# Kernel tuning notes

Measured on AMD Instinct MI355X. Metric: run time of the kernel, lower is better.

Reference implementation:

```python
import jax, jax.numpy as jnp
import numpy as np

HEAD_SIZE = 128
LAMBDA_INIT = 0.8
FILL = 1e-09  # the module fills masked positions with 1e-9 (not -inf); reproduce faithfully


def setup_inputs() -> dict:
    key = jax.random.key(0)
    ks = jax.random.split(key, 12)
    B, T, C = 8, 2048, 1024
    q = jax.random.normal(ks[0], (B, T, C), dtype=jnp.float32)
    k = jax.random.normal(ks[1], (B, T, C), dtype=jnp.float32)
    v = jax.random.normal(ks[2], (B, T, C), dtype=jnp.float32)
    pad_mask = jax.random.randint(ks[3], (B, T), 0, 2, dtype=jnp.int32)
    scale = 1.0 / np.sqrt(C)
    Wq = jax.random.normal(ks[4], (C, 2 * HEAD_SIZE), dtype=jnp.float32) * scale
    Wk = jax.random.normal(ks[5], (C, 2 * HEAD_SIZE), dtype=jnp.float32) * scale
    Wv = jax.random.normal(ks[6], (C, HEAD_SIZE), dtype=jnp.float32) * scale
    lq1 = jax.random.normal(ks[7], (HEAD_SIZE,), dtype=jnp.float32)
    lk1 = jax.random.normal(ks[8], (HEAD_SIZE,), dtype=jnp.float32)
    lq2 = jax.random.normal(ks[9], (HEAD_SIZE,), dtype=jnp.float32)
    lk2 = jax.random.normal(ks[10], (HEAD_SIZE,), dtype=jnp.float32)
    return {"q": q, "k": k, "v": v, "pad_mask": pad_mask,
            "Wq": Wq, "Wk": Wk, "Wv": Wv,
            "lq1": lq1, "lk1": lk1, "lq2": lq2, "lk2": lk2}


def reference(q, k, v, pad_mask, Wq, Wk, Wv, lq1, lk1, lq2, lk2):
    B, T_q, C = q.shape
    T_k = k.shape[1]
    Q = q @ Wq                      # [B, Tq, 2*hs]
    K = k @ Wk                      # [B, Tk, 2*hs]
    V = v @ Wv                      # [B, Tk, ho]
    Q1, Q2 = jnp.split(Q, 2, axis=-1)
    K1, K2 = jnp.split(K, 2, axis=-1)
    s1 = jnp.einsum("bqd,bkd->bqk", Q1, K1)
    s2 = jnp.einsum("bqd,bkd->bqk", Q2, K2)
    # causal mask: tril(ones, diagonal=1) == 0 -> fill (note diagonal=1, one lookahead)
    causal_fill = jnp.tril(jnp.ones((T_q, T_k), dtype=bool), 1) == False
    s1 = jnp.where(causal_fill[None], FILL, s1)
    s2 = jnp.where(causal_fill[None], FILL, s2)
    # pad mask broadcast over the KEY axis per query row (as in original)
    pad_fill = (pad_mask == 1)[:, :, None]  # [B, Tq, 1]
    s1 = jnp.where(pad_fill, FILL, s1)
    s2 = jnp.where(pad_fill, FILL, s2)
    scale = HEAD_SIZE ** (-0.5)
    lbd = jnp.exp(jnp.dot(lq1, lk1)) - jnp.exp(jnp.dot(lq2, lk2)) + LAMBDA_INIT
    attn = jax.nn.softmax(s1 * scale, axis=-1) - lbd * jax.nn.softmax(s2 * scale, axis=-1)
    return attn @ V                 # [B, Tq, ho]
```

## Files before the change

kernel.cpp:

```cpp
#include <hip/hip_runtime.h>
#include <math.h>


#define T_SEQ 2048
#define NB 8
#define CDIM 1024
#define HS 128

constexpr float SCALE = 0.08838834764831845f;

typedef float f32x4 __attribute__((ext_vector_type(4)));
typedef __bf16 bf16x8 __attribute__((ext_vector_type(8)));
typedef unsigned int u32;

#define MFMA16 __builtin_amdgcn_mfma_f32_16x16x32_bf16

__device__ __forceinline__ void gld16(const void* g, void* l) {
  __builtin_amdgcn_global_load_lds(
      (const __attribute__((address_space(1))) u32*)g,
      (__attribute__((address_space(3))) u32*)l, 16, 0, 0);
}

__device__ __forceinline__ void wg_barrier_lds() {
  asm volatile("s_waitcnt lgkmcnt(0)" ::: "memory");
  __builtin_amdgcn_s_barrier();
  __builtin_amdgcn_sched_barrier(0);
}

__device__ __forceinline__ bf16x8 cvt8(f32x4 lo, f32x4 hi) {
  bf16x8 r;
  r[0] = (__bf16)lo.x; r[1] = (__bf16)lo.y; r[2] = (__bf16)lo.z; r[3] = (__bf16)lo.w;
  r[4] = (__bf16)hi.x; r[5] = (__bf16)hi.y; r[6] = (__bf16)hi.z; r[7] = (__bf16)hi.w;
  return r;
}

__global__ __launch_bounds__(128) void lambda_kernel(
    const float* __restrict__ lq1, const float* __restrict__ lk1,
    const float* __restrict__ lq2, const float* __restrict__ lk2,
    float* __restrict__ lbd) {
  __shared__ float r1[128], r2[128];
  int t = threadIdx.x;
  r1[t] = lq1[t] * lk1[t];
  r2[t] = lq2[t] * lk2[t];
  __syncthreads();
  for (int s = 64; s > 0; s >>= 1) {
    if (t < s) { r1[t] += r1[t + s]; r2[t] += r2[t + s]; }
    __syncthreads();
  }
  if (t == 0) *lbd = expf(r1[0]) - expf(r2[0]) + 0.8f;
}

__global__ __launch_bounds__(256) void pack_w(
    const float* __restrict__ Wq, const float* __restrict__ Wk,
    const float* __restrict__ Wv, __bf16* __restrict__ Wp) {
  int nt = blockIdx.x;
  const float* W; int colbase, N;
  if (nt < 16)      { W = Wq; colbase = nt * 16;        N = 256; }
  else if (nt < 32) { W = Wk; colbase = (nt - 16) * 16; N = 256; }
  else              { W = Wv; colbase = (nt - 32) * 16; N = 128; }
  int tid = threadIdx.x;
#pragma unroll
  for (int i = 0; i < 8; ++i) {
    int u = tid + 256 * i;
    int ks = u >> 6, lane = u & 63;
    int l15 = lane & 15, quad = lane >> 4;
    bf16x8 pk;
#pragma unroll
    for (int j = 0; j < 8; ++j)
      pk[j] = (__bf16)W[(size_t)(ks * 32 + quad * 8 + j) * N + colbase + l15];
    *(bf16x8*)(Wp + ((size_t)(nt * 32 + ks) * 64 + lane) * 8) = pk;
  }
}

template<int NT, int NTG>
__device__ __forceinline__ void proj_body(
    const float* __restrict__ Ablk, const __bf16* __restrict__ Wp,
    __bf16* __restrict__ outp, __bf16* __restrict__ Vt,
    int rows0, char* smem) {
  constexpr int NT2 = NT / 2;
  float*  sA = (float*)smem;
  __bf16* sB = (__bf16*)(smem + 16384);
  const int tid = threadIdx.x;
  const int lane = tid & 63, wave = tid >> 6;
  const int wr = wave >> 1, wc = wave & 1;
  const int l15 = lane & 15, quad = lane >> 4;
  const int arow = lane >> 3;
  const int ac16 = (lane & 7) ^ arow;

  f32x4 acc0[NT2], acc1[NT2];
#pragma unroll
  for (int j = 0; j < NT2; ++j) {
    acc0[j] = (f32x4){0.f, 0.f, 0.f, 0.f};
    acc1[j] = (f32x4){0.f, 0.f, 0.f, 0.f};
  }

  auto stage_ks = [&](int ks, int buf) {
    const float* gA = Ablk + ks * 32;
    float* lA = sA + buf * 2048;
#pragma unroll
    for (int i = 0; i < 2; ++i) {
      int li = wave * 2 + i;
      gld16(gA + (size_t)(li * 8 + arow) * CDIM + ac16 * 4, lA + li * 256);
    }
    __bf16* lB = sB + buf * 8192;
#pragma unroll
    for (int i = 0; i < 4; ++i) {
      int ntl = i * 4 + wave;
      if (ntl < NT)
        gld16(Wp + ((size_t)((NTG + ntl) * 32 + ks) * 64 + lane) * 8,
              lB + ntl * 512);
    }
  };

  stage_ks(0, 0);
  for (int ks = 0; ks < 32; ++ks) {
    const int buf = ks & 1;
    __syncthreads();
    const float* lA = sA + buf * 2048;
    int r0 = wr * 32 + l15;
    f32x4 lo0 = *(const f32x4*)(lA + r0 * 32 + (((quad * 2)     ^ (l15 & 7)) * 4));
    f32x4 hi0 = *(const f32x4*)(lA + r0 * 32 + (((quad * 2 + 1) ^ (l15 & 7)) * 4));
    bf16x8 af0 = cvt8(lo0, hi0);
    int r1 = r0 + 16;
    f32x4 lo1 = *(const f32x4*)(lA + r1 * 32 + (((quad * 2)     ^ (l15 & 7)) * 4));
    f32x4 hi1 = *(const f32x4*)(lA + r1 * 32 + (((quad * 2 + 1) ^ (l15 & 7)) * 4));
    bf16x8 af1 = cvt8(lo1, hi1);
    if (ks < 31) stage_ks(ks + 1, buf ^ 1);
    const __bf16* lB = sB + buf * 8192;
#pragma unroll
    for (int nt = 0; nt < NT2; ++nt) {
      bf16x8 bf = *(const bf16x8*)(lB + (wc * NT2 + nt) * 512 + lane * 8);
      acc0[nt] = MFMA16(af0, bf, acc0[nt], 0, 0, 0);
      acc1[nt] = MFMA16(af1, bf, acc1[nt], 0, 0, 0);
    }
  }

  __syncthreads();
  constexpr int N = NT * 16;
  constexpr int TS = N + 8;
  __bf16* tile = (__bf16*)smem;
#pragma unroll
  for (int ntl = 0; ntl < NT2; ++ntl) {
    f32x4 a0 = acc0[ntl];
    f32x4 a1 = acc1[ntl];
#pragma unroll
    for (int r = 0; r < 4; ++r) {
      tile[(wr * 32 + quad * 4 + r) * TS + (wc * NT2 + ntl) * 16 + l15] = (__bf16)a0[r];
      tile[(wr * 32 + 16 + quad * 4 + r) * TS + (wc * NT2 + ntl) * 16 + l15] = (__bf16)a1[r];
    }
  }
  __syncthreads();
  constexpr int CPR = N / 8;
#pragma unroll
  for (int i = 0; i < (64 * CPR) / 256; ++i) {
    int u = tid + 256 * i;
    int row = u / CPR, c8 = u % CPR;
    bf16x8 val = *(const bf16x8*)(tile + row * TS + c8 * 8);
    *(bf16x8*)(outp + (size_t)(rows0 + row) * N + c8 * 8) = val;
  }
  if constexpr (NT == 8) {
    int b = rows0 >> 11, t0 = rows0 & 2047;
#pragma unroll
    for (int i = 0; i < 4; ++i) {
      int u = tid + 256 * i;
      int tc = u & 7, c = u >> 3;
      bf16x8 pk;
#pragma unroll
      for (int j = 0; j < 8; ++j) pk[j] = tile[(tc * 8 + j) * TS + c];
      *(bf16x8*)(Vt + ((size_t)(b * 128 + c)) * T_SEQ + t0 + tc * 8) = pk;
    }
  }
}

__global__ __launch_bounds__(256, 3) void proj_mfma(
    const float* __restrict__ qin, const float* __restrict__ kin,
    const float* __restrict__ vin, const __bf16* __restrict__ Wp,
    __bf16* __restrict__ Qo, __bf16* __restrict__ Ko,
    __bf16* __restrict__ Vo, __bf16* __restrict__ Vt) {
  __shared__ char smem[49152];
  const int blk = blockIdx.x;
  const int rows0 = (blk & 255) * 64;
  if (blk < 256)
    proj_body<16, 0>(qin + (size_t)rows0 * CDIM, Wp, Qo, nullptr, rows0, smem);
  else if (blk < 512)
    proj_body<16, 16>(kin + (size_t)rows0 * CDIM, Wp, Ko, nullptr, rows0, smem);
  else
    proj_body<8, 32>(vin + (size_t)rows0 * CDIM, Wp, Vo, Vt, rows0, smem);
}

#define VCH 64
#define VCS 32
__global__ __launch_bounds__(128) void vcsum_a(const __bf16* __restrict__ V,
                                               float* __restrict__ csum) {
  int blk = blockIdx.x; int b = blk >> 6, ch = blk & 63;
  int c = threadIdx.x;
  const __bf16* vp = V + ((size_t)b * T_SEQ + ch * VCS) * HS + c;
  float s = 0.f;
#pragma unroll 4
  for (int t = 0; t < VCS; ++t) s += (float)vp[(size_t)t * HS];
  csum[(size_t)blk * HS + c] = s;
}

__global__ __launch_bounds__(128) void vcsum_b(const __bf16* __restrict__ V,
                                               const float* __restrict__ csum,
                                               float* __restrict__ cum) {
  int blk = blockIdx.x; int b = blk >> 6, ch = blk & 63;
  int c = threadIdx.x;
  float run = 0.f;
  for (int j = 0; j < ch; ++j) run += csum[(size_t)(b * VCH + j) * HS + c];
  const __bf16* vp = V + ((size_t)b * T_SEQ + ch * VCS) * HS + c;
  float* cp = cum + ((size_t)b * (T_SEQ + 1) + ch * VCS) * HS + c;
  if (ch == 0) cp[0] = 0.f;
#pragma unroll 4
  for (int t = 0; t < VCS; ++t) {
    run += (float)vp[(size_t)t * HS];
    cp[(size_t)(t + 1) * HS] = run;
  }
}

__global__ __launch_bounds__(512, 2) void attn_mfma(
    const __bf16* __restrict__ Q, const __bf16* __restrict__ K,
    const __bf16* __restrict__ Vt, const float* __restrict__ cum,
    const int* __restrict__ pad, const float* __restrict__ lbdp,
    float* __restrict__ out) {
  __shared__ __bf16 sQ[32 * 264];
  __shared__ __bf16 sK[2][64 * 256];
  __shared__ __bf16 sP[2][2][32 * 72];
  __shared__ float zb[2][32][64];
  __shared__ float zfin[2][32];

  const int tid = threadIdx.x;
  const int lane = tid & 63, wave = tid >> 6;
  const int wm = wave >> 2, wk = wave & 3;
  const int l15 = lane & 15, quad = lane >> 4;

  const int p = blockIdx.x;
  const int b = p & 7;
  const int ti = 63 - (p >> 3);
  const int q0 = ti * 32;
  const float lbd = *lbdp;
  const __bf16* Qb = Q + (size_t)b * T_SEQ * 256;
  const __bf16* Kb = K + (size_t)b * T_SEQ * 256;
  const __bf16* Vtb = Vt + (size_t)b * HS * T_SEQ;
  const float* cumb = cum + (size_t)b * (T_SEQ + 1) * HS;
  const float pc = (1.f - lbd) * (1.f / (float)T_SEQ);

  const int lastkey = q0 + 32;
  const int nkt = (min(lastkey, T_SEQ - 1) >> 6) + 1;

  auto stageK = [&](int k0, int sbuf) {
#pragma unroll
    for (int i = 0; i < 4; ++i) {
      int u = i * 512 + tid;
      int row = u >> 5, c = u & 31;
      int cg = (c & 24) | ((c ^ row) & 7);
      gld16(Kb + (size_t)(k0 + row) * 256 + cg * 8,
            &sK[sbuf][(size_t)(i * 512 + wave * 64) * 8]);
    }
  };

  stageK(0, 0);
#pragma unroll
  for (int i = 0; i < 2; ++i) {
    int c = tid + 512 * i;
    int row = c >> 5, c16 = c & 31;
    *(f32x4*)(&sQ[row * 264 + c16 * 8]) =
        *(const f32x4*)(Qb + (size_t)(q0 + row) * 256 + c16 * 8);
  }
  __syncthreads();

  bf16x8 qf[2][4];
  {
    const int row = wm * 16 + l15;
#pragma unroll
    for (int pl = 0; pl < 2; ++pl)
#pragma unroll
      for (int s = 0; s < 4; ++s)
        qf[pl][s] = *(const bf16x8*)(&sQ[row * 264 + pl * 128 + s * 32 + quad * 8]);
  }

  f32x4 O[2][2];
#pragma unroll
  for (int i = 0; i < 2; ++i)
#pragma unroll
    for (int j = 0; j < 2; ++j) O[i][j] = (f32x4){0.f, 0.f, 0.f, 0.f};
  float z[2][4] = {};

  const int kr = wk * 16 + l15;

  for (int kt = 0; kt < nkt; ++kt) {
    const int k0 = kt << 6;
    const int buf = kt & 1;
    const bool needmask = (k0 + 63 > q0 + 1);

    bf16x8 vf[2][2];
#pragma unroll
    for (int nt = 0; nt < 2; ++nt)
#pragma unroll
      for (int ks = 0; ks < 2; ++ks)
        vf[nt][ks] = *(const bf16x8*)(Vtb + (size_t)(wk * 32 + nt * 16 + l15) * T_SEQ +
                                      k0 + ks * 32 + quad * 8);
    if (kt + 1 < nkt) stageK(k0 + 64, buf ^ 1);

    f32x4 S[2];
#pragma unroll
    for (int mat = 0; mat < 2; ++mat) {
      S[mat] = (f32x4){0.f, 0.f, 0.f, 0.f};
#pragma unroll
      for (int s = 0; s < 4; ++s) {
        int cd = mat * 16 + s * 4 + quad;
        int slot = (cd & 24) | ((cd ^ kr) & 7);
        bf16x8 kfrag = *(const bf16x8*)(&sK[buf][(size_t)kr * 256 + slot * 8]);
        S[mat] = MFMA16(qf[mat][s], kfrag, S[mat], 0, 0, 0);
      }
    }

    const int rowl = wm * 16 + quad * 4;
    const int keyg = k0 + kr;
#pragma unroll
    for (int mat = 0; mat < 2; ++mat)
#pragma unroll
      for (int r = 0; r < 4; ++r) {
        float pv;
        if (needmask) {
          int rowg = q0 + rowl + r;
          pv = (keyg <= rowg + 1) ? __expf(S[mat][r] * SCALE) : 0.f;
        } else {
          pv = __expf(S[mat][r] * SCALE);
        }
        z[mat][r] += pv;
        sP[buf][mat][(rowl + r) * 72 + kr] = (__bf16)pv;
      }
    wg_barrier_lds();

#pragma unroll
    for (int ks = 0; ks < 2; ++ks) {
      bf16x8 pf0 = *(const bf16x8*)(&sP[buf][0][(wm * 16 + l15) * 72 + ks * 32 + quad * 8]);
      bf16x8 pf1 = *(const bf16x8*)(&sP[buf][1][(wm * 16 + l15) * 72 + ks * 32 + quad * 8]);
#pragma unroll
      for (int nt = 0; nt < 2; ++nt) {
        O[0][nt] = MFMA16(pf0, vf[nt][ks], O[0][nt], 0, 0, 0);
        O[1][nt] = MFMA16(pf1, vf[nt][ks], O[1][nt], 0, 0, 0);
      }
    }
    __syncthreads();
  }

#pragma unroll
  for (int mat = 0; mat < 2; ++mat)
#pragma unroll
    for (int r = 0; r < 4; ++r)
      zb[mat][wm * 16 + quad * 4 + r][wk * 16 + l15] = z[mat][r];
  __syncthreads();
  if (tid < 64) {
    int mat = tid >> 5, row = tid & 31;
    float s = 0.f;
#pragma unroll
    for (int j = 0; j < 64; ++j) s += zb[mat][row][(j + tid) & 63];
    zfin[mat][row] = s;
  }
  __syncthreads();

#pragma unroll
  for (int r = 0; r < 4; ++r) {
    const int rowl = wm * 16 + quad * 4 + r;
    const int rowg = q0 + rowl;
    const int nallow = min(rowg + 2, T_SEQ);
    const float nmask = (float)(T_SEQ - nallow);
    const float Z1 = zfin[0][rowl] + nmask;
    const float Z2 = zfin[1][rowl] + nmask;
    const float i1 = 1.f / Z1, i2 = lbd / Z2;
    const float tc = i1 - i2;
    const bool isp = (pad[b * T_SEQ + rowg] == 1);
#pragma unroll
    for (int nt = 0; nt < 2; ++nt) {
      const int col = wk * 32 + nt * 16 + l15;
      const float ct = cumb[(size_t)T_SEQ * HS + col];
      const float cn = cumb[(size_t)nallow * HS + col];
      float val = isp ? (pc * ct)
                      : (O[0][nt][r] * i1 - O[1][nt][r] * i2 + tc * (ct - cn));
      out[((size_t)b * T_SEQ + rowg) * HS + col] = val;
    }
  }
}

extern "C" void kernel_launch(void* const* d_in, const int* in_sizes, int n_in,
                              void* d_out, int out_size, void* d_ws, size_t ws_size,
                              hipStream_t stream) {
  (void)in_sizes; (void)n_in; (void)out_size; (void)ws_size;
  const float* q   = (const float*)d_in[0];
  const float* k   = (const float*)d_in[1];
  const float* v   = (const float*)d_in[2];
  const int*   pm  = (const int*)d_in[3];
  const float* Wq  = (const float*)d_in[4];
  const float* Wk  = (const float*)d_in[5];
  const float* Wv  = (const float*)d_in[6];
  const float* lq1 = (const float*)d_in[7];
  const float* lk1 = (const float*)d_in[8];
  const float* lq2 = (const float*)d_in[9];
  const float* lk2 = (const float*)d_in[10];
  float* out = (float*)d_out;
  char* ws = (char*)d_ws;

  float*  lbd  = (float*)ws;
  __bf16* Wp   = (__bf16*)(ws + 16);
  __bf16* Qp   = (__bf16*)(ws + 16 + 1310720);
  __bf16* Kp   = Qp + (size_t)NB * T_SEQ * 256;
  __bf16* Vp   = Kp + (size_t)NB * T_SEQ * 256;
  __bf16* Vt   = Vp + (size_t)NB * T_SEQ * HS;
  float*  cum  = (float*)(Vt + (size_t)NB * T_SEQ * HS);
  float*  csum = cum + (size_t)NB * (T_SEQ + 1) * HS;

  lambda_kernel<<<dim3(1), dim3(128), 0, stream>>>(lq1, lk1, lq2, lk2, lbd);
  pack_w<<<dim3(40), dim3(256), 0, stream>>>(Wq, Wk, Wv, Wp);
  proj_mfma<<<dim3(768), dim3(256), 0, stream>>>(q, k, v, Wp, Qp, Kp, Vp, Vt);
  vcsum_a<<<dim3(512), dim3(128), 0, stream>>>(Vp, csum);
  vcsum_b<<<dim3(512), dim3(128), 0, stream>>>(Vp, csum, cum);
  attn_mfma<<<dim3(512), dim3(512), 0, stream>>>(Qp, Kp, Vt, cum, pm, lbd, out);
}
```

Measured before the change: 340.9 us.

## Triple-buffer projection GEMM loads with explicit vmcnt waits

Converts the projection kernel's double-buffered LDS staging into a three-slot ring that prefetches two K-steps ahead. Each iteration waits on vmcnt counts with raw s_waitcnt plus s_barrier instead of __syncthreads. The goal is to hide more global-load latency behind the MFMA work. In exchange, LDS grows to 72KB and occupancy drops from 3 to 2 blocks per CU, and correctness now relies on hand-counted outstanding loads.

```diff
diff --git a/kernel.cpp b/kernel.cpp
--- a/kernel.cpp
+++ b/kernel.cpp
@@ -79,7 +79,7 @@
     int rows0, char* smem) {
   constexpr int NT2 = NT / 2;
   float*  sA = (float*)smem;
-  __bf16* sB = (__bf16*)(smem + 16384);
+  __bf16* sB = (__bf16*)(smem + 24576);
   const int tid = threadIdx.x;
   const int lane = tid & 63, wave = tid >> 6;
   const int wr = wave >> 1, wc = wave & 1;
@@ -94,15 +94,15 @@
     acc1[j] = (f32x4){0.f, 0.f, 0.f, 0.f};
   }
 
-  auto stage_ks = [&](int ks, int buf) {
+  auto stage_ks = [&](int ks, int slot) {
     const float* gA = Ablk + ks * 32;
-    float* lA = sA + buf * 2048;
+    float* lA = sA + slot * 2048;
 #pragma unroll
     for (int i = 0; i < 2; ++i) {
       int li = wave * 2 + i;
       gld16(gA + (size_t)(li * 8 + arow) * CDIM + ac16 * 4, lA + li * 256);
     }
-    __bf16* lB = sB + buf * 8192;
+    __bf16* lB = sB + slot * 8192;
 #pragma unroll
     for (int i = 0; i < 4; ++i) {
       int ntl = i * 4 + wave;
@@ -113,10 +113,21 @@
   };
 
   stage_ks(0, 0);
+  stage_ks(1, 1);
+  int slot = 0;
   for (int ks = 0; ks < 32; ++ks) {
-    const int buf = ks & 1;
-    __syncthreads();
-    const float* lA = sA + buf * 2048;
+    if (ks < 31) {
+      if constexpr (NT == 16)
+        asm volatile("s_waitcnt vmcnt(6) lgkmcnt(0)" ::: "memory");
+      else
+        asm volatile("s_waitcnt vmcnt(4) lgkmcnt(0)" ::: "memory");
+    } else {
+      asm volatile("s_waitcnt vmcnt(0) lgkmcnt(0)" ::: "memory");
+    }
+    __builtin_amdgcn_s_barrier();
+    __builtin_amdgcn_sched_barrier(0);
+
+    const float* lA = sA + slot * 2048;
     int r0 = wr * 32 + l15;
     f32x4 lo0 = *(const f32x4*)(lA + r0 * 32 + (((quad * 2)     ^ (l15 & 7)) * 4));
     f32x4 hi0 = *(const f32x4*)(lA + r0 * 32 + (((quad * 2 + 1) ^ (l15 & 7)) * 4));
@@ -125,14 +136,20 @@
     f32x4 lo1 = *(const f32x4*)(lA + r1 * 32 + (((quad * 2)     ^ (l15 & 7)) * 4));
     f32x4 hi1 = *(const f32x4*)(lA + r1 * 32 + (((quad * 2 + 1) ^ (l15 & 7)) * 4));
     bf16x8 af1 = cvt8(lo1, hi1);
-    if (ks < 31) stage_ks(ks + 1, buf ^ 1);
-    const __bf16* lB = sB + buf * 8192;
+
+    if (ks + 2 < 32) {
+      int slot2 = slot + 2; if (slot2 >= 3) slot2 -= 3;
+      stage_ks(ks + 2, slot2);
+    }
+
+    const __bf16* lB = sB + slot * 8192;
 #pragma unroll
     for (int nt = 0; nt < NT2; ++nt) {
       bf16x8 bf = *(const bf16x8*)(lB + (wc * NT2 + nt) * 512 + lane * 8);
       acc0[nt] = MFMA16(af0, bf, acc0[nt], 0, 0, 0);
       acc1[nt] = MFMA16(af1, bf, acc1[nt], 0, 0, 0);
     }
+    ++slot; if (slot == 3) slot = 0;
   }
 
   __syncthreads();
@@ -172,12 +189,12 @@
   }
 }
 
-__global__ __launch_bounds__(256, 3) void proj_mfma(
+__global__ __launch_bounds__(256, 2) void proj_mfma(
     const float* __restrict__ qin, const float* __restrict__ kin,
     const float* __restrict__ vin, const __bf16* __restrict__ Wp,
     __bf16* __restrict__ Qo, __bf16* __restrict__ Ko,
     __bf16* __restrict__ Vo, __bf16* __restrict__ Vt) {
-  __shared__ char smem[49152];
+  __shared__ char smem[73728];
   const int blk = blockIdx.x;
   const int rows0 = (blk & 255) * 64;
   if (blk < 256)
```

Result: faster. 330.3 us (-3.1%).

## Halve projection row tile and stage A in 128-wide K chunks

Applied to the files above, without the earlier changes.

The projection kernel now processes 32 rows per block instead of 64, doubling the grid to 1536 blocks. The fp32 activation tile is staged in 128-column chunks, double-buffered every four k-steps, while the weight tile is still staged every step. Each wave now runs one MFMA row tile instead of two. The aim is better load balance across CUs and fewer, larger activation loads. The cost is twice as many weight fetches per output row, a 64KB LDS footprint, and occupancy lowered to 2 blocks per CU.

```diff
diff --git a/kernel.cpp b/kernel.cpp
--- a/kernel.cpp
+++ b/kernel.cpp
@@ -79,30 +79,31 @@
     int rows0, char* smem) {
   constexpr int NT2 = NT / 2;
   float*  sA = (float*)smem;
-  __bf16* sB = (__bf16*)(smem + 16384);
+  __bf16* sB = (__bf16*)(smem + 32768);
   const int tid = threadIdx.x;
   const int lane = tid & 63, wave = tid >> 6;
   const int wr = wave >> 1, wc = wave & 1;
   const int l15 = lane & 15, quad = lane >> 4;
-  const int arow = lane >> 3;
-  const int ac16 = (lane & 7) ^ arow;
-
-  f32x4 acc0[NT2], acc1[NT2];
-#pragma unroll
-  for (int j = 0; j < NT2; ++j) {
-    acc0[j] = (f32x4){0.f, 0.f, 0.f, 0.f};
-    acc1[j] = (f32x4){0.f, 0.f, 0.f, 0.f};
-  }
-
-  auto stage_ks = [&](int ks, int buf) {
-    const float* gA = Ablk + ks * 32;
-    float* lA = sA + buf * 2048;
-#pragma unroll
-    for (int i = 0; i < 2; ++i) {
-      int li = wave * 2 + i;
-      gld16(gA + (size_t)(li * 8 + arow) * CDIM + ac16 * 4, lA + li * 256);
-    }
-    __bf16* lB = sB + buf * 8192;
+  const int lhalf = lane >> 5;
+  const int l31 = lane & 31;
+
+  f32x4 acc[NT2];
+#pragma unroll
+  for (int j = 0; j < NT2; ++j) acc[j] = (f32x4){0.f, 0.f, 0.f, 0.f};
+
+  auto stage_A = [&](int g, int abuf) {
+    float* lA = sA + abuf * 4096;
+    const float* gA = Ablk + g * 128;
+#pragma unroll
+    for (int i = 0; i < 4; ++i) {
+      int rp = wave * 4 + i;
+      int row = rp * 2 + lhalf;
+      int ch = l31 ^ (row & 31);
+      gld16(gA + (size_t)row * CDIM + ch * 4, lA + rp * 256);
+    }
+  };
+  auto stage_B = [&](int ks, int bbuf) {
+    __bf16* lB = sB + bbuf * 8192;
 #pragma unroll
     for (int i = 0; i < 4; ++i) {
       int ntl = i * 4 + wave;
@@ -112,26 +113,28 @@
     }
   };
 
-  stage_ks(0, 0);
+  stage_A(0, 0);
+  stage_B(0, 0);
   for (int ks = 0; ks < 32; ++ks) {
-    const int buf = ks & 1;
+    const int abuf = (ks >> 2) & 1;
+    const int bbuf = ks & 1;
     __syncthreads();
-    const float* lA = sA + buf * 2048;
-    int r0 = wr * 32 + l15;
-    f32x4 lo0 = *(const f32x4*)(lA + r0 * 32 + (((quad * 2)     ^ (l15 & 7)) * 4));
-    f32x4 hi0 = *(const f32x4*)(lA + r0 * 32 + (((quad * 2 + 1) ^ (l15 & 7)) * 4));
-    bf16x8 af0 = cvt8(lo0, hi0);
-    int r1 = r0 + 16;
-    f32x4 lo1 = *(const f32x4*)(lA + r1 * 32 + (((quad * 2)     ^ (l15 & 7)) * 4));
-    f32x4 hi1 = *(const f32x4*)(lA + r1 * 32 + (((quad * 2 + 1) ^ (l15 & 7)) * 4));
-    bf16x8 af1 = cvt8(lo1, hi1);
-    if (ks < 31) stage_ks(ks + 1, buf ^ 1);
-    const __bf16* lB = sB + buf * 8192;
+
+    const float* lA = sA + abuf * 4096;
+    const int row = wr * 16 + l15;
+    const int g0 = (ks & 3) * 8 + quad * 2;
+    f32x4 lo = *(const f32x4*)(lA + row * 128 + ((g0 ^ row) & 31) * 4);
+    f32x4 hi = *(const f32x4*)(lA + row * 128 + (((g0 + 1) ^ row) & 31) * 4);
+    bf16x8 af = cvt8(lo, hi);
+
+    if ((ks & 3) == 0 && ks + 4 < 32) stage_A((ks >> 2) + 1, abuf ^ 1);
+    if (ks + 1 < 32) stage_B(ks + 1, bbuf ^ 1);
+
+    const __bf16* lB = sB + bbuf * 8192;
 #pragma unroll
     for (int nt = 0; nt < NT2; ++nt) {
       bf16x8 bf = *(const bf16x8*)(lB + (wc * NT2 + nt) * 512 + lane * 8);
-      acc0[nt] = MFMA16(af0, bf, acc0[nt], 0, 0, 0);
-      acc1[nt] = MFMA16(af1, bf, acc1[nt], 0, 0, 0);
+      acc[nt] = MFMA16(af, bf, acc[nt], 0, 0, 0);
     }
   }
 
@@ -140,19 +143,16 @@
   constexpr int TS = N + 8;
   __bf16* tile = (__bf16*)smem;
 #pragma unroll
-  for (int ntl = 0; ntl < NT2; ++ntl) {
-    f32x4 a0 = acc0[ntl];
-    f32x4 a1 = acc1[ntl];
-#pragma unroll
-    for (int r = 0; r < 4; ++r) {
-      tile[(wr * 32 + quad * 4 + r) * TS + (wc * NT2 + ntl) * 16 + l15] = (__bf16)a0[r];
-      tile[(wr * 32 + 16 + quad * 4 + r) * TS + (wc * NT2 + ntl) * 16 + l15] = (__bf16)a1[r];
-    }
+  for (int nt = 0; nt < NT2; ++nt) {
+    f32x4 a = acc[nt];
+#pragma unroll
+    for (int r = 0; r < 4; ++r)
+      tile[(wr * 16 + quad * 4 + r) * TS + (wc * NT2 + nt) * 16 + l15] = (__bf16)a[r];
   }
   __syncthreads();
   constexpr int CPR = N / 8;
 #pragma unroll
-  for (int i = 0; i < (64 * CPR) / 256; ++i) {
+  for (int i = 0; i < (32 * CPR) / 256; ++i) {
     int u = tid + 256 * i;
     int row = u / CPR, c8 = u % CPR;
     bf16x8 val = *(const bf16x8*)(tile + row * TS + c8 * 8);
@@ -161,9 +161,9 @@
   if constexpr (NT == 8) {
     int b = rows0 >> 11, t0 = rows0 & 2047;
 #pragma unroll
-    for (int i = 0; i < 4; ++i) {
+    for (int i = 0; i < 2; ++i) {
       int u = tid + 256 * i;
-      int tc = u & 7, c = u >> 3;
+      int tc = u & 3, c = u >> 2;
       bf16x8 pk;
 #pragma unroll
       for (int j = 0; j < 8; ++j) pk[j] = tile[(tc * 8 + j) * TS + c];
@@ -172,17 +172,17 @@
   }
 }
 
-__global__ __launch_bounds__(256, 3) void proj_mfma(
+__global__ __launch_bounds__(256, 2) void proj_mfma(
     const float* __restrict__ qin, const float* __restrict__ kin,
     const float* __restrict__ vin, const __bf16* __restrict__ Wp,
     __bf16* __restrict__ Qo, __bf16* __restrict__ Ko,
     __bf16* __restrict__ Vo, __bf16* __restrict__ Vt) {
-  __shared__ char smem[49152];
+  __shared__ char smem[65536];
   const int blk = blockIdx.x;
-  const int rows0 = (blk & 255) * 64;
-  if (blk < 256)
+  const int rows0 = (blk & 511) * 32;
+  if (blk < 512)
     proj_body<16, 0>(qin + (size_t)rows0 * CDIM, Wp, Qo, nullptr, rows0, smem);
-  else if (blk < 512)
+  else if (blk < 1024)
     proj_body<16, 16>(kin + (size_t)rows0 * CDIM, Wp, Ko, nullptr, rows0, smem);
   else
     proj_body<8, 32>(vin + (size_t)rows0 * CDIM, Wp, Vo, Vt, rows0, smem);
@@ -413,7 +413,7 @@
 
   lambda_kernel<<<dim3(1), dim3(128), 0, stream>>>(lq1, lk1, lq2, lk2, lbd);
   pack_w<<<dim3(40), dim3(256), 0, stream>>>(Wq, Wk, Wv, Wp);
-  proj_mfma<<<dim3(768), dim3(256), 0, stream>>>(q, k, v, Wp, Qp, Kp, Vp, Vt);
+  proj_mfma<<<dim3(1536), dim3(256), 0, stream>>>(q, k, v, Wp, Qp, Kp, Vp, Vt);
   vcsum_a<<<dim3(512), dim3(128), 0, stream>>>(Vp, csum);
   vcsum_b<<<dim3(512), dim3(128), 0, stream>>>(Vp, csum, cum);
   attn_mfma<<<dim3(512), dim3(512), 0, stream>>>(Qp, Kp, Vt, cum, pm, lbd, out);
```

New measurement: 337.4 us. About the same (-1.0%).
